# Kernel tuning notes

Measured on AMD Instinct MI355X. Metric: run time of the kernel, lower is better.

## Reference

```python
import jax, jax.numpy as jnp
import numpy as np

TAU = 10.0
N, D = 4096, 8192  # batch, feature dim (D >= N required by the original indexing)
NUM_CLASSES = 100


def setup_inputs() -> dict:
    key = jax.random.key(0)
    k1, k2 = jax.random.split(key)
    embeddings = jax.random.normal(k1, (N, D), dtype=jnp.float32)
    labels = jax.random.randint(k2, (N,), 0, NUM_CLASSES, dtype=jnp.int64)
    return {"embeddings": embeddings, "labels": labels}


def reference(embeddings, labels):
    # Faithful to the original (buggy) torch math:
    # inner_product[i, d] = exp(emb[i, d]**2 / tau)  (trailing singleton dim dropped)
    n = embeddings.shape[0]
    A = jnp.exp(embeddings * embeddings / TAU)          # [N, D]
    # denominator_i = sum_d A[i, d] - A[i, i]
    denom = jnp.sum(A, axis=1) - jnp.diagonal(A)[:n]    # [N]
    # numerator terms: exp(A[i, j] / tau) for j in batch indices (j < N <= D)
    B = jnp.exp(A[:, :n] / TAU)                          # [N, N]
    same = labels[:, None] == labels[None, :]            # [N, N]
    mask = same & ~jnp.eye(n, dtype=bool)
    counts = jnp.sum(mask, axis=1).astype(embeddings.dtype)   # misma_clase per i
    suma = jnp.sum(jnp.where(mask, B, jnp.zeros((), B.dtype)), axis=1) / denom  # [N]
    return jnp.sum(jnp.log(suma / counts))
```

## Files before the change

### kernel.cpp

```cpp
#include <hip/hip_runtime.h>

static constexpr int N = 4096;
static constexpr int D = 8192;
static constexpr int BLOCK = 256;

__global__ __launch_bounds__(BLOCK) void supcon_rows(
    const float* __restrict__ emb,
    const int* __restrict__ labels,
    float* __restrict__ row_out)
{
    const int row = blockIdx.x;
    const int tid = threadIdx.x;
    const int lab_i = labels[row];
    const float4* rowp = reinterpret_cast<const float4*>(emb + (size_t)row * D);
    const int4* labp = reinterpret_cast<const int4*>(labels);

    float4 v[8];
    #pragma unroll
    for (int it = 0; it < 8; ++it)
        v[it] = rowp[tid + it * BLOCK];
    int4 lj[4];
    #pragma unroll
    for (int it = 0; it < 4; ++it)
        lj[it] = labp[tid + it * BLOCK];

    float denom = 0.f, ssum = 0.f, diag = 0.f, fcnt = 0.f;

    #pragma unroll
    for (int it = 0; it < 4; ++it) {
        const int j0 = (tid + it * BLOCK) * 4;
        float xs[4] = {v[it].x, v[it].y, v[it].z, v[it].w};
        int   ls[4] = {lj[it].x, lj[it].y, lj[it].z, lj[it].w};
        #pragma unroll
        for (int k = 0; k < 4; ++k) {
            float a = __expf(xs[k] * xs[k] * 0.1f);
            denom += a;
            float b = __expf(a * 0.1f);
            bool match = (ls[k] == lab_i) && (j0 + k != row);
            ssum += match ? b : 0.f;
            fcnt += match ? 1.f : 0.f;
            diag += (j0 + k == row) ? a : 0.f;
        }
    }
    #pragma unroll
    for (int it = 4; it < 8; ++it) {
        float xs[4] = {v[it].x, v[it].y, v[it].z, v[it].w};
        #pragma unroll
        for (int k = 0; k < 4; ++k)
            denom += __expf(xs[k] * xs[k] * 0.1f);
    }

    #pragma unroll
    for (int off = 32; off > 0; off >>= 1) {
        denom += __shfl_down(denom, off);
        ssum  += __shfl_down(ssum,  off);
        diag  += __shfl_down(diag,  off);
        fcnt  += __shfl_down(fcnt,  off);
    }

    __shared__ float s_red[4][4];
    const int wave = tid >> 6;
    if ((tid & 63) == 0) {
        s_red[0][wave] = denom;
        s_red[1][wave] = ssum;
        s_red[2][wave] = diag;
        s_red[3][wave] = fcnt;
    }
    __syncthreads();
    if (tid == 0) {
        float dn = 0.f, sv = 0.f, dg = 0.f, c = 0.f;
        #pragma unroll
        for (int w = 0; w < 4; ++w) {
            dn += s_red[0][w]; sv += s_red[1][w]; dg += s_red[2][w]; c += s_red[3][w];
        }
        dn -= dg;
        row_out[row] = __logf(sv) - __logf(dn) - __logf(c);
    }
}

__global__ __launch_bounds__(1024) void reduce_rows(
    const float* __restrict__ row_vals, float* __restrict__ out)
{
    const int tid = threadIdx.x;
    float4 x = reinterpret_cast<const float4*>(row_vals)[tid];
    float s = x.x + x.y + x.z + x.w;
    #pragma unroll
    for (int off = 32; off > 0; off >>= 1)
        s += __shfl_down(s, off);
    __shared__ float sb[16];
    if ((tid & 63) == 0) sb[tid >> 6] = s;
    __syncthreads();
    if (tid == 0) {
        float t = 0.f;
        #pragma unroll
        for (int w = 0; w < 16; ++w) t += sb[w];
        *out = t;
    }
}

extern "C" void kernel_launch(void* const* d_in, const int* in_sizes, int n_in,
                              void* d_out, int out_size, void* d_ws, size_t ws_size,
                              hipStream_t stream) {
    const float* emb  = (const float*)d_in[0];
    const int* labels = (const int*)d_in[1];
    float* out        = (float*)d_out;
    float* row_vals   = (float*)d_ws;

    supcon_rows<<<dim3(N), dim3(BLOCK), 0, stream>>>(emb, labels, row_vals);
    reduce_rows<<<dim3(1), dim3(1024), 0, stream>>>(row_vals, out);
}
```

Baseline: 187.8 us.

## Assign one wavefront per row and drop block-level shared-memory reduction

Each 256-thread block now handles four rows, with one 64-lane wavefront per row, so the row reduction needs only wave shuffles and no LDS or __syncthreads. Each wave streams its 32 KB row in two chunks of eight float4 loads. This removes block synchronisation and shared-memory traffic. In exchange there is less memory-level parallelism per row and more loop iterations per thread.

```diff
diff --git a/kernel.cpp b/kernel.cpp
--- a/kernel.cpp
+++ b/kernel.cpp
@@ -3,51 +3,63 @@
 static constexpr int N = 4096;
 static constexpr int D = 8192;
 static constexpr int BLOCK = 256;
+static constexpr int ROWS_PER_BLOCK = 4;
 
 __global__ __launch_bounds__(BLOCK) void supcon_rows(
     const float* __restrict__ emb,
     const int* __restrict__ labels,
     float* __restrict__ row_out)
 {
-    const int row = blockIdx.x;
-    const int tid = threadIdx.x;
+    const int wave = threadIdx.x >> 6;
+    const int lane = threadIdx.x & 63;
+    const int row  = blockIdx.x * ROWS_PER_BLOCK + wave;
     const int lab_i = labels[row];
+
     const float4* rowp = reinterpret_cast<const float4*>(emb + (size_t)row * D);
-    const int4* labp = reinterpret_cast<const int4*>(labels);
-
-    float4 v[8];
-    #pragma unroll
-    for (int it = 0; it < 8; ++it)
-        v[it] = rowp[tid + it * BLOCK];
-    int4 lj[4];
-    #pragma unroll
-    for (int it = 0; it < 4; ++it)
-        lj[it] = labp[tid + it * BLOCK];
+    const int4*   labp = reinterpret_cast<const int4*>(labels);
 
     float denom = 0.f, ssum = 0.f, diag = 0.f, fcnt = 0.f;
 
     #pragma unroll
-    for (int it = 0; it < 4; ++it) {
-        const int j0 = (tid + it * BLOCK) * 4;
-        float xs[4] = {v[it].x, v[it].y, v[it].z, v[it].w};
-        int   ls[4] = {lj[it].x, lj[it].y, lj[it].z, lj[it].w};
+    for (int c = 0; c < 2; ++c) {
+        float4 v[8]; int4 lj[8];
         #pragma unroll
-        for (int k = 0; k < 4; ++k) {
-            float a = __expf(xs[k] * xs[k] * 0.1f);
-            denom += a;
-            float b = __expf(a * 0.1f);
-            bool match = (ls[k] == lab_i) && (j0 + k != row);
-            ssum += match ? b : 0.f;
-            fcnt += match ? 1.f : 0.f;
-            diag += (j0 + k == row) ? a : 0.f;
+        for (int i = 0; i < 8; ++i) {
+            const int idx = (c * 8 + i) * 64 + lane;
+            v[i]  = rowp[idx];
+            lj[i] = labp[idx];
+        }
+        #pragma unroll
+        for (int i = 0; i < 8; ++i) {
+            const int j0 = ((c * 8 + i) * 64 + lane) * 4;
+            const float xs[4] = {v[i].x, v[i].y, v[i].z, v[i].w};
+            const int   ls[4] = {lj[i].x, lj[i].y, lj[i].z, lj[i].w};
+            #pragma unroll
+            for (int k = 0; k < 4; ++k) {
+                float a = __expf(xs[k] * xs[k] * 0.1f);
+                denom += a;
+                float b = __expf(a * 0.1f);
+                bool match = (ls[k] == lab_i) && (j0 + k != row);
+                ssum += match ? b : 0.f;
+                fcnt += match ? 1.f : 0.f;
+                diag += (j0 + k == row) ? a : 0.f;
+            }
         }
     }
+
     #pragma unroll
-    for (int it = 4; it < 8; ++it) {
-        float xs[4] = {v[it].x, v[it].y, v[it].z, v[it].w};
+    for (int c = 0; c < 2; ++c) {
+        float4 v[8];
         #pragma unroll
-        for (int k = 0; k < 4; ++k)
-            denom += __expf(xs[k] * xs[k] * 0.1f);
+        for (int i = 0; i < 8; ++i)
+            v[i] = rowp[1024 + (c * 8 + i) * 64 + lane];
+        #pragma unroll
+        for (int i = 0; i < 8; ++i) {
+            denom += __expf(v[i].x * v[i].x * 0.1f);
+            denom += __expf(v[i].y * v[i].y * 0.1f);
+            denom += __expf(v[i].z * v[i].z * 0.1f);
+            denom += __expf(v[i].w * v[i].w * 0.1f);
+        }
     }
 
     #pragma unroll
@@ -57,24 +69,9 @@
         diag  += __shfl_down(diag,  off);
         fcnt  += __shfl_down(fcnt,  off);
     }
-
-    __shared__ float s_red[4][4];
-    const int wave = tid >> 6;
-    if ((tid & 63) == 0) {
-        s_red[0][wave] = denom;
-        s_red[1][wave] = ssum;
-        s_red[2][wave] = diag;
-        s_red[3][wave] = fcnt;
-    }
-    __syncthreads();
-    if (tid == 0) {
-        float dn = 0.f, sv = 0.f, dg = 0.f, c = 0.f;
-        #pragma unroll
-        for (int w = 0; w < 4; ++w) {
-            dn += s_red[0][w]; sv += s_red[1][w]; dg += s_red[2][w]; c += s_red[3][w];
-        }
-        dn -= dg;
-        row_out[row] = __logf(sv) - __logf(dn) - __logf(c);
+    if (lane == 0) {
+        const float dn = denom - diag;
+        row_out[row] = __logf(ssum) - __logf(dn) - __logf(fcnt);
     }
 }
 
@@ -106,6 +103,6 @@
     float* out        = (float*)d_out;
     float* row_vals   = (float*)d_ws;
 
-    supcon_rows<<<dim3(N), dim3(BLOCK), 0, stream>>>(emb, labels, row_vals);
+    supcon_rows<<<dim3(N / ROWS_PER_BLOCK), dim3(BLOCK), 0, stream>>>(emb, labels, row_vals);
     reduce_rows<<<dim3(1), dim3(1024), 0, stream>>>(row_vals, out);
 }
```

New measurement: 192.5 us. +2.5%, slower.
